# Performance work log

Hardware: AMD Instinct MI355X
Metric: run time of the kernel (lower is better)

The kernel has to match this reference:

```python
import jax, jax.numpy as jnp
import numpy as np

N_NODES = 100000


def sage_conv(x, src, dst, Wl, bl, Wr):
    # PyG SAGEConv (aggr='mean'): out = lin_l(mean_{j in N(i)} x_j) + lin_r(x_i)
    msg = x[src]                                                   # [E, d] gather
    agg = jax.ops.segment_sum(msg, dst, num_segments=N_NODES)      # [N, d]
    cnt = jax.ops.segment_sum(jnp.ones((src.shape[0], 1), x.dtype), dst,
                              num_segments=N_NODES)                # [N, 1]
    mean = agg / jnp.maximum(cnt, 1.0)
    return mean @ Wl + bl + x @ Wr


def setup_inputs() -> dict:
    key = jax.random.key(0)
    ks = jax.random.split(key, 9)
    N, E, D_IN = N_NODES, 3200000, 64
    x = jax.random.normal(ks[0], (N, D_IN), dtype=jnp.float32)
    edge_index = jax.random.randint(ks[1], (2, E), 0, N, dtype=jnp.int64)

    def glorot(k, fan_in, fan_out):
        lim = float(np.sqrt(6.0 / (fan_in + fan_out)))
        return jax.random.uniform(k, (fan_in, fan_out), jnp.float32, -lim, lim)

    return {
        "x": x,
        "edge_index": edge_index,
        "W1l": glorot(ks[2], D_IN, 64), "b1": jnp.zeros((64,), jnp.float32),
        "W1r": glorot(ks[3], D_IN, 64),
        "W2l": glorot(ks[4], 64, 32), "b2": jnp.zeros((32,), jnp.float32),
        "W2r": glorot(ks[5], 64, 32),
        "W3l": glorot(ks[6], 32, 1), "b3": jnp.zeros((1,), jnp.float32),
        "W3r": glorot(ks[7], 32, 1),
    }


def reference(x, edge_index, W1l, b1, W1r, W2l, b2, W2r, W3l, b3, W3r):
    src, dst = edge_index[0], edge_index[1]
    h = jax.nn.relu(sage_conv(x, src, dst, W1l, b1, W1r))   # dropout: eval mode (identity)
    h = jax.nn.relu(sage_conv(h, src, dst, W2l, b2, W2r))
    h = sage_conv(h, src, dst, W3l, b3, W3r)
    return jax.nn.sigmoid(h)                                # [N, 1]
```

## Files before the change

### kernel.cpp

```cpp
#include <hip/hip_runtime.h>
#include <math.h>

#define NN 100000
#define NB 391
#define BT 8192
#define CAP 12288

typedef float vfloat2 __attribute__((ext_vector_type(2)));
typedef short short8 __attribute__((ext_vector_type(8)));
typedef float floatx4 __attribute__((ext_vector_type(4)));

__device__ __forceinline__ unsigned short f2bf(float f) {
    unsigned int u = __float_as_uint(f);
    u += 0x7fffu + ((u >> 16) & 1u);
    return (unsigned short)(u >> 16);
}

__device__ __forceinline__ unsigned char f2fp8(float f) {
    const int p = __builtin_amdgcn_cvt_pk_fp8_f32(f, f, 0, false);
    return (unsigned char)(p & 0xFF);
}
template <bool HI>
__device__ __forceinline__ vfloat2 fp8pk2(unsigned int w) {
    return __builtin_amdgcn_cvt_pk_f32_fp8((int)w, HI);
}

template <int D_IN, int CL, int CR, int NPB, int FUSE_IN>
__global__ void __launch_bounds__(256)
mlp_mfma_kernel(const float* __restrict__ in0,
                const float* __restrict__ in1,
                const float* __restrict__ Wl,
                const float* __restrict__ Wr,
                const float* __restrict__ bias,
                unsigned char* __restrict__ yout,
                float* __restrict__ zout,
                int n_nodes) {
    constexpr int COLS = CL + CR;
    constexpr int CT = COLS / 16;
    constexpr int KT = D_IN / 32;
    constexpr int NT = NPB / 16;
    constexpr int KG = D_IN / 8;
    __shared__ short sA[NT * KT * 64 * 8];
    __shared__ short sB[CT * KT * 64 * 8];
    __shared__ float sBias[CR];
    const int t = threadIdx.x;
    const int node0 = blockIdx.x * NPB;

    for (int i = t; i < NPB * KG; i += 256) {
        const int nl = i / KG, kg = i % KG;
        const int n = node0 + nl;
        float v[8];
        if (n < n_nodes) {
            const float4* p = (const float4*)(in0 + (long long)n * D_IN + kg * 8);
            float4 a0 = p[0], a1 = p[1];
            if (FUSE_IN) {
                const float4* q = (const float4*)(in1 + (long long)n * D_IN + kg * 8);
                const float4 b0 = q[0], b1 = q[1];
                a0.x = fmaxf(a0.x + b0.x, 0.f); a0.y = fmaxf(a0.y + b0.y, 0.f);
                a0.z = fmaxf(a0.z + b0.z, 0.f); a0.w = fmaxf(a0.w + b0.w, 0.f);
                a1.x = fmaxf(a1.x + b1.x, 0.f); a1.y = fmaxf(a1.y + b1.y, 0.f);
                a1.z = fmaxf(a1.z + b1.z, 0.f); a1.w = fmaxf(a1.w + b1.w, 0.f);
            }
            v[0] = a0.x; v[1] = a0.y; v[2] = a0.z; v[3] = a0.w;
            v[4] = a1.x; v[5] = a1.y; v[6] = a1.z; v[7] = a1.w;
        } else {
#pragma unroll
            for (int j = 0; j < 8; ++j) v[j] = 0.f;
        }
        short8 s;
#pragma unroll
        for (int j = 0; j < 8; ++j) s[j] = (short)f2bf(v[j]);
        const int nt = nl >> 4, m = nl & 15, kt = kg >> 2, quad = kg & 3;
        ((short8*)sA)[(nt * KT + kt) * 64 + quad * 16 + m] = s;
    }
    for (int i = t; i < CT * KT * 64; i += 256) {
        const int ct = i / (KT * 64);
        const int rem = i % (KT * 64);
        const int kt = rem / 64, L = rem % 64;
        const int c = ct * 16 + (L & 15);
        const int k0 = kt * 32 + (L >> 4) * 8;
        short8 s;
#pragma unroll
        for (int j = 0; j < 8; ++j) {
            const int k = k0 + j;
            const float w = (c < CL) ? Wl[k * CL + c] : Wr[k * CR + (c - CL)];
            s[j] = (short)f2bf(w);
        }
        ((short8*)sB)[i] = s;
    }
    for (int i = t; i < CR; i += 256) sBias[i] = bias[i];
    __syncthreads();

    const int w = t >> 6, lane = t & 63;
    short8 Bf[CT][KT];
#pragma unroll
    for (int ct = 0; ct < CT; ++ct)
#pragma unroll
        for (int kt = 0; kt < KT; ++kt)
            Bf[ct][kt] = ((short8*)sB)[(ct * KT + kt) * 64 + lane];
    const int col = lane & 15, quad = lane >> 4;
#pragma unroll
    for (int nti = 0; nti < NT / 4; ++nti) {
        const int nt = w * (NT / 4) + nti;
        short8 A[KT];
#pragma unroll
        for (int kt = 0; kt < KT; ++kt)
            A[kt] = ((short8*)sA)[(nt * KT + kt) * 64 + lane];
        const int nodeb = node0 + nt * 16 + quad * 4;
#pragma unroll
        for (int ct = 0; ct < CT; ++ct) {
            floatx4 acc = {0.f, 0.f, 0.f, 0.f};
#pragma unroll
            for (int kt = 0; kt < KT; ++kt)
                acc = __builtin_amdgcn_mfma_f32_16x16x32_bf16(A[kt], Bf[ct][kt], acc, 0, 0, 0);
            const int gc = ct * 16 + col;
#pragma unroll
            for (int r = 0; r < 4; ++r) {
                const int node = nodeb + r;
                if (node < n_nodes) {
                    if (gc < CL) yout[(long long)node * CL + gc] = f2fp8(acc[r]);
                    else zout[(long long)node * CR + (gc - CL)] = acc[r] + sBias[gc - CL];
                }
            }
        }
    }
}

template <int D_IN>
__global__ void __launch_bounds__(256)
mlp3_kernel(const float* __restrict__ mean,
            const float* __restrict__ z,
            const float* __restrict__ W3l,
            const float* __restrict__ W3r,
            const float* __restrict__ b3,
            float* __restrict__ y,
            float* __restrict__ z3, int n_nodes) {
    __shared__ float swl[D_IN], swr[D_IN];
    const int t = threadIdx.x;
    if (t < D_IN) { swl[t] = W3l[t]; swr[t] = W3r[t]; }
    __syncthreads();
    const int n = blockIdx.x * 256 + t;
    if (n >= n_nodes) return;
    const float4* pm = (const float4*)(mean + (long long)n * D_IN);
    const float4* pz = (const float4*)(z + (long long)n * D_IN);
    float accl = 0.f, accr = 0.f;
#pragma unroll
    for (int q = 0; q < D_IN / 4; ++q) {
        const float4 m4 = pm[q];
        const float4 z4 = pz[q];
        const float h0 = fmaxf(m4.x + z4.x, 0.f);
        const float h1 = fmaxf(m4.y + z4.y, 0.f);
        const float h2 = fmaxf(m4.z + z4.z, 0.f);
        const float h3 = fmaxf(m4.w + z4.w, 0.f);
        accl += h0 * swl[4 * q] + h1 * swl[4 * q + 1] + h2 * swl[4 * q + 2] + h3 * swl[4 * q + 3];
        accr += h0 * swr[4 * q] + h1 * swr[4 * q + 1] + h2 * swr[4 * q + 2] + h3 * swr[4 * q + 3];
    }
    y[n] = accl;
    z3[n] = accr + b3[0];
}

__global__ void sigmoid_out_kernel(const float* __restrict__ mean,
                                   const float* __restrict__ z,
                                   float* __restrict__ out, int n) {
    const int i = blockIdx.x * 256 + threadIdx.x;
    if (i < n) out[i] = 1.0f / (1.0f + expf(-(mean[i] + z[i])));
}

__global__ void bucket_hist_kernel(const int* __restrict__ dst,
                                   int* __restrict__ bcnt, int n_edges) {
    __shared__ int lh[NB];
    for (int i = threadIdx.x; i < NB; i += 256) lh[i] = 0;
    __syncthreads();
    const int stride = gridDim.x * 256;
    for (int i = blockIdx.x * 256 + threadIdx.x; i < n_edges; i += stride)
        atomicAdd(&lh[dst[i] >> 8], 1);
    __syncthreads();
    for (int i = threadIdx.x; i < NB; i += 256)
        if (lh[i]) atomicAdd(&bcnt[i], lh[i]);
}

__global__ void __launch_bounds__(512)
bucket_scan_kernel(const int* __restrict__ bcnt, int* __restrict__ boffs,
                   int* __restrict__ bcursor) {
    __shared__ int s[512];
    const int t = threadIdx.x;
    const int v = (t < NB) ? bcnt[t] : 0;
    s[t] = v;
    __syncthreads();
    for (int off = 1; off < 512; off <<= 1) {
        const int tmp = (t >= off) ? s[t - off] : 0;
        __syncthreads();
        s[t] += tmp;
        __syncthreads();
    }
    const int excl = s[t] - v;
    if (t <= NB) boffs[t] = excl;
    if (t < NB) bcursor[t] = excl;
}

__global__ void __launch_bounds__(512)
bin_edges_kernel(const int* __restrict__ src, const int* __restrict__ dst,
                 int* __restrict__ bcursor, unsigned int* __restrict__ binned,
                 int n_edges) {
    __shared__ unsigned int stage[BT];
    __shared__ unsigned short sbkt[BT];
    __shared__ int lhist[512], lscan[512], lstart[512], gbase[512], lcur[512];
    const int t = threadIdx.x;
    const int e0 = blockIdx.x * BT;
    const int count = min(BT, n_edges - e0);
    lhist[t] = 0;
    __syncthreads();
    for (int i = t; i < count; i += 512) atomicAdd(&lhist[dst[e0 + i] >> 8], 1);
    __syncthreads();
    const int v = lhist[t];
    lscan[t] = v;
    __syncthreads();
    for (int off = 1; off < 512; off <<= 1) {
        const int tmp = (t >= off) ? lscan[t - off] : 0;
        __syncthreads();
        lscan[t] += tmp;
        __syncthreads();
    }
    const int excl = lscan[t] - v;
    lstart[t] = excl;
    lcur[t] = excl;
    if (t < NB && v > 0) gbase[t] = atomicAdd(&bcursor[t], v);
    __syncthreads();
    for (int i = t; i < count; i += 512) {
        const int d = dst[e0 + i];
        const int b = d >> 8;
        const int p = atomicAdd(&lcur[b], 1);
        stage[p] = (unsigned int)src[e0 + i] | ((unsigned int)(d & 255) << 17);
        sbkt[p] = (unsigned short)b;
    }
    __syncthreads();
    for (int i = t; i < count; i += 512) {
        const int b = sbkt[i];
        binned[gbase[b] + (i - lstart[b])] = stage[i];
    }
}

__global__ void __launch_bounds__(1024)
csr_sort_kernel(const unsigned int* __restrict__ binned,
                const int* __restrict__ boffs,
                int* __restrict__ ssrc, int* __restrict__ row_ptr,
                float* __restrict__ inv_deg, int n_nodes, int n_edges) {
    __shared__ int stage[CAP];
    __shared__ int hist[256];
    __shared__ int lexcl[256];
    __shared__ int lcur[256];
    const int t = threadIdx.x;
    const int b = blockIdx.x;
    const int s0 = boffs[b], s1 = boffs[b + 1];
    const int count = s1 - s0;
    if (t < 256) hist[t] = 0;
    __syncthreads();
    for (int i = t; i < count; i += 1024)
        atomicAdd(&hist[binned[s0 + i] >> 17], 1);
    __syncthreads();
    if (t < 256) lexcl[t] = hist[t];
    __syncthreads();
    for (int off = 1; off < 256; off <<= 1) {
        int tmp = 0;
        if (t < 256 && t >= off) tmp = lexcl[t - off];
        __syncthreads();
        if (t < 256) lexcl[t] += tmp;
        __syncthreads();
    }
    if (t < 256) {
        const int excl = lexcl[t] - hist[t];
        lcur[t] = excl;
        const int n = (b << 8) + t;
        if (n < n_nodes) {
            row_ptr[n] = s0 + excl;
            inv_deg[n] = 1.0f / (float)max(hist[t], 1);
        }
    }
    if (b == NB - 1 && t == 0) row_ptr[n_nodes] = n_edges;
    __syncthreads();
    for (int i = t; i < count; i += 1024) {
        const unsigned int v = binned[s0 + i];
        const int p = atomicAdd(&lcur[v >> 17], 1);
        if (p < CAP) stage[p] = (int)(v & 0x1FFFFu);
    }
    __syncthreads();
    for (int i = t; i < count; i += 1024) ssrc[s0 + i] = stage[i];
}

template <int D>
__global__ void agg_mean_fp8_kernel(const unsigned int* __restrict__ yb,
                                    const int* __restrict__ row_ptr,
                                    const int* __restrict__ ssrc,
                                    const float* __restrict__ inv_deg,
                                    float* __restrict__ mean, int n_nodes) {
    constexpr int G = D / 16;
    constexpr int NPB = 256 / G;
    const int g = threadIdx.x / G;
    const int lane = threadIdx.x % G;
    const int n = blockIdx.x * NPB + g;
    if (n >= n_nodes) return;
    const int s0 = row_ptr[n], s1 = row_ptr[n + 1];
    const uint4* yv = (const uint4*)yb;
    float acc[16];
#pragma unroll
    for (int i = 0; i < 16; ++i) acc[i] = 0.f;
    int e = s0;
    for (; e + 4 <= s1; e += 4) {
        uint4 v[4];
        v[0] = yv[(long long)ssrc[e] * G + lane];
        v[1] = yv[(long long)ssrc[e + 1] * G + lane];
        v[2] = yv[(long long)ssrc[e + 2] * G + lane];
        v[3] = yv[(long long)ssrc[e + 3] * G + lane];
#pragma unroll
        for (int q = 0; q < 4; ++q) {
            const unsigned int wx = v[q].x, wy = v[q].y, wz = v[q].z, ww = v[q].w;
            vfloat2 p;
            p = fp8pk2<false>(wx); acc[0]  += p.x; acc[1]  += p.y;
            p = fp8pk2<true>(wx);  acc[2]  += p.x; acc[3]  += p.y;
            p = fp8pk2<false>(wy); acc[4]  += p.x; acc[5]  += p.y;
            p = fp8pk2<true>(wy);  acc[6]  += p.x; acc[7]  += p.y;
            p = fp8pk2<false>(wz); acc[8]  += p.x; acc[9]  += p.y;
            p = fp8pk2<true>(wz);  acc[10] += p.x; acc[11] += p.y;
            p = fp8pk2<false>(ww); acc[12] += p.x; acc[13] += p.y;
            p = fp8pk2<true>(ww);  acc[14] += p.x; acc[15] += p.y;
        }
    }
    for (; e < s1; ++e) {
        const uint4 v = yv[(long long)ssrc[e] * G + lane];
        vfloat2 p;
        p = fp8pk2<false>(v.x); acc[0]  += p.x; acc[1]  += p.y;
        p = fp8pk2<true>(v.x);  acc[2]  += p.x; acc[3]  += p.y;
        p = fp8pk2<false>(v.y); acc[4]  += p.x; acc[5]  += p.y;
        p = fp8pk2<true>(v.y);  acc[6]  += p.x; acc[7]  += p.y;
        p = fp8pk2<false>(v.z); acc[8]  += p.x; acc[9]  += p.y;
        p = fp8pk2<true>(v.z);  acc[10] += p.x; acc[11] += p.y;
        p = fp8pk2<false>(v.w); acc[12] += p.x; acc[13] += p.y;
        p = fp8pk2<true>(v.w);  acc[14] += p.x; acc[15] += p.y;
    }
    const float inv = inv_deg[n];
    float4* mv = (float4*)mean;
    const long long base = (long long)n * (D / 4) + lane * 4;
#pragma unroll
    for (int q = 0; q < 4; ++q)
        mv[base + q] = make_float4(acc[4 * q] * inv, acc[4 * q + 1] * inv,
                                   acc[4 * q + 2] * inv, acc[4 * q + 3] * inv);
}

__global__ void agg_mean_d1_kernel(const float* __restrict__ y,
                                   const int* __restrict__ row_ptr,
                                   const int* __restrict__ ssrc,
                                   const float* __restrict__ inv_deg,
                                   float* __restrict__ mean, int n_nodes) {
    const int wave = threadIdx.x >> 6;
    const int lane = threadIdx.x & 63;
    const int n = blockIdx.x * 4 + wave;
    if (n >= n_nodes) return;
    const int s0 = row_ptr[n], s1 = row_ptr[n + 1];
    float acc = 0.f;
    for (int e = s0 + lane; e < s1; e += 64) acc += y[ssrc[e]];
    for (int off = 32; off > 0; off >>= 1) acc += __shfl_down(acc, off, 64);
    if (lane == 0) mean[n] = acc * inv_deg[n];
}

extern "C" void kernel_launch(void* const* d_in, const int* in_sizes, int n_in,
                              void* d_out, int out_size, void* d_ws, size_t ws_size,
                              hipStream_t stream) {
    const float* x = (const float*)d_in[0];
    const int* edge_index = (const int*)d_in[1];
    const float* W1l = (const float*)d_in[2];
    const float* b1  = (const float*)d_in[3];
    const float* W1r = (const float*)d_in[4];
    const float* W2l = (const float*)d_in[5];
    const float* b2  = (const float*)d_in[6];
    const float* W2r = (const float*)d_in[7];
    const float* W3l = (const float*)d_in[8];
    const float* b3  = (const float*)d_in[9];
    const float* W3r = (const float*)d_in[10];
    float* out = (float*)d_out;

    const int E = in_sizes[1] / 2;
    const int* src = edge_index;
    const int* dst = edge_index + E;

    float* bufY    = (float*)d_ws;
    float* meanB   = bufY + 32LL * NN;
    float* z1      = meanB + 64LL * NN;
    float* z2      = z1 + 64LL * NN;
    float* z3      = z2 + 32LL * NN;
    float* inv_deg = z3 + NN;
    int* bcnt      = (int*)(inv_deg + NN);
    int* boffs     = bcnt + NB;
    int* bcursor   = boffs + NB + 1;
    int* row_ptr   = bcursor + NB;
    int* ssrc      = row_ptr + NN + 1;
    unsigned int* binned = (unsigned int*)z1;

    const int ntiles = (E + BT - 1) / BT;

    (void)hipMemsetAsync(bcnt, 0, NB * sizeof(int), stream);
    bucket_hist_kernel<<<512, 256, 0, stream>>>(dst, bcnt, E);
    bucket_scan_kernel<<<1, 512, 0, stream>>>(bcnt, boffs, bcursor);
    bin_edges_kernel<<<ntiles, 512, 0, stream>>>(src, dst, bcursor, binned, E);
    csr_sort_kernel<<<NB, 1024, 0, stream>>>(binned, boffs, ssrc, row_ptr, inv_deg, NN, E);

    mlp_mfma_kernel<64, 64, 64, 128, 0><<<(NN + 127) / 128, 256, 0, stream>>>(
        x, nullptr, W1l, W1r, b1, (unsigned char*)bufY, z1, NN);
    agg_mean_fp8_kernel<64><<<(NN + 63) / 64, 256, 0, stream>>>(
        (const unsigned int*)bufY, row_ptr, ssrc, inv_deg, meanB, NN);

    mlp_mfma_kernel<64, 32, 32, 128, 1><<<(NN + 127) / 128, 256, 0, stream>>>(
        meanB, z1, W2l, W2r, b2, (unsigned char*)bufY, z2, NN);
    agg_mean_fp8_kernel<32><<<(NN + 127) / 128, 256, 0, stream>>>(
        (const unsigned int*)bufY, row_ptr, ssrc, inv_deg, meanB, NN);

    mlp3_kernel<32><<<(NN + 255) / 256, 256, 0, stream>>>(
        meanB, z2, W3l, W3r, b3, bufY, z3, NN);
    agg_mean_d1_kernel<<<(NN + 3) / 4, 256, 0, stream>>>(
        bufY, row_ptr, ssrc, inv_deg, meanB, NN);
    sigmoid_out_kernel<<<(NN + 255) / 256, 256, 0, stream>>>(meanB, z3, out, NN);
}
```

Baseline: 301.8 us.

## Split layer-1 aggregation into planar halves and fuse tail kernels

```diff
diff --git a/kernel.cpp b/kernel.cpp
--- a/kernel.cpp
+++ b/kernel.cpp
@@ -25,7 +25,19 @@
     return __builtin_amdgcn_cvt_pk_f32_fp8((int)w, HI);
 }
 
-template <int D_IN, int CL, int CR, int NPB, int FUSE_IN>
+__device__ __forceinline__ void fp8x16_acc(const uint4 v, float* acc) {
+    vfloat2 p;
+    p = fp8pk2<false>(v.x); acc[0]  += p.x; acc[1]  += p.y;
+    p = fp8pk2<true>(v.x);  acc[2]  += p.x; acc[3]  += p.y;
+    p = fp8pk2<false>(v.y); acc[4]  += p.x; acc[5]  += p.y;
+    p = fp8pk2<true>(v.y);  acc[6]  += p.x; acc[7]  += p.y;
+    p = fp8pk2<false>(v.z); acc[8]  += p.x; acc[9]  += p.y;
+    p = fp8pk2<true>(v.z);  acc[10] += p.x; acc[11] += p.y;
+    p = fp8pk2<false>(v.w); acc[12] += p.x; acc[13] += p.y;
+    p = fp8pk2<true>(v.w);  acc[14] += p.x; acc[15] += p.y;
+}
+
+template <int D_IN, int CL, int CR, int NPB, int FUSE_IN, int YPLANAR>
 __global__ void __launch_bounds__(256)
 mlp_mfma_kernel(const float* __restrict__ in0,
                 const float* __restrict__ in1,
@@ -118,52 +130,147 @@
             for (int r = 0; r < 4; ++r) {
                 const int node = nodeb + r;
                 if (node < n_nodes) {
-                    if (gc < CL) yout[(long long)node * CL + gc] = f2fp8(acc[r]);
-                    else zout[(long long)node * CR + (gc - CL)] = acc[r] + sBias[gc - CL];
+                    if (gc < CL) {
+                        if (YPLANAR) {
+                            const int plane = gc >> 5;
+                            yout[(long long)plane * NN * 32 + (long long)node * 32 + (gc & 31)] = f2fp8(acc[r]);
+                        } else {
+                            yout[(long long)node * CL + gc] = f2fp8(acc[r]);
+                        }
+                    } else {
+                        zout[(long long)node * CR + (gc - CL)] = acc[r] + sBias[gc - CL];
+                    }
                 }
             }
         }
     }
 }
 
-template <int D_IN>
+template <int HALF>
+__global__ void __launch_bounds__(128)
+agg64_half_kernel(const unsigned int* __restrict__ yb,
+                  const int* __restrict__ row_ptr,
+                  const int* __restrict__ ssrc,
+                  const float* __restrict__ inv_deg,
+                  float* __restrict__ mean, int n_nodes) {
+    const int g = threadIdx.x >> 1;
+    const int lane = threadIdx.x & 1;
+    const int n = blockIdx.x * 64 + g;
+    if (n >= n_nodes) return;
+    const int s0 = row_ptr[n], s1 = row_ptr[n + 1];
+    const uint4* yv = (const uint4*)yb;
+    const long long pbase = (long long)HALF * NN * 2;
+    float acc[16];
+#pragma unroll
+    for (int i = 0; i < 16; ++i) acc[i] = 0.f;
+    int e = s0;
+    for (; e + 4 <= s1; e += 4) {
+        const int i0 = __builtin_nontemporal_load(ssrc + e);
+        const int i1 = __builtin_nontemporal_load(ssrc + e + 1);
+        const int i2 = __builtin_nontemporal_load(ssrc + e + 2);
+        const int i3 = __builtin_nontemporal_load(ssrc + e + 3);
+        const uint4 v0 = yv[pbase + (long long)i0 * 2 + lane];
+        const uint4 v1 = yv[pbase + (long long)i1 * 2 + lane];
+        const uint4 v2 = yv[pbase + (long long)i2 * 2 + lane];
+        const uint4 v3 = yv[pbase + (long long)i3 * 2 + lane];
+        fp8x16_acc(v0, acc); fp8x16_acc(v1, acc);
+        fp8x16_acc(v2, acc); fp8x16_acc(v3, acc);
+    }
+    for (; e < s1; ++e) {
+        const int i0 = __builtin_nontemporal_load(ssrc + e);
+        fp8x16_acc(yv[pbase + (long long)i0 * 2 + lane], acc);
+    }
+    const float inv = inv_deg[n];
+    float4* mv = (float4*)mean;
+    const long long base = (long long)n * 16 + HALF * 8 + lane * 4;
+#pragma unroll
+    for (int q = 0; q < 4; ++q)
+        mv[base + q] = make_float4(acc[4 * q] * inv, acc[4 * q + 1] * inv,
+                                   acc[4 * q + 2] * inv, acc[4 * q + 3] * inv);
+}
+
 __global__ void __launch_bounds__(256)
-mlp3_kernel(const float* __restrict__ mean,
-            const float* __restrict__ z,
-            const float* __restrict__ W3l,
-            const float* __restrict__ W3r,
-            const float* __restrict__ b3,
-            float* __restrict__ y,
-            float* __restrict__ z3, int n_nodes) {
-    __shared__ float swl[D_IN], swr[D_IN];
-    const int t = threadIdx.x;
-    if (t < D_IN) { swl[t] = W3l[t]; swr[t] = W3r[t]; }
-    __syncthreads();
-    const int n = blockIdx.x * 256 + t;
+agg32_mlp3_kernel(const unsigned int* __restrict__ yb,
+                  const int* __restrict__ row_ptr,
+                  const int* __restrict__ ssrc,
+                  const float* __restrict__ inv_deg,
+                  const float* __restrict__ z2,
+                  const float* __restrict__ W3l,
+                  const float* __restrict__ W3r,
+                  const float* __restrict__ b3,
+                  float* __restrict__ y3,
+                  float* __restrict__ z3, int n_nodes) {
+    const int g = threadIdx.x >> 1;
+    const int lane = threadIdx.x & 1;
+    const int n = blockIdx.x * 128 + g;
     if (n >= n_nodes) return;
-    const float4* pm = (const float4*)(mean + (long long)n * D_IN);
-    const float4* pz = (const float4*)(z + (long long)n * D_IN);
+    float wl[16], wr[16];
+#pragma unroll
+    for (int i = 0; i < 16; ++i) {
+        wl[i] = W3l[lane * 16 + i];
+        wr[i] = W3r[lane * 16 + i];
+    }
+    const int s0 = row_ptr[n], s1 = row_ptr[n + 1];
+    const uint4* yv = (const uint4*)yb;
+    float acc[16];
+#pragma unroll
+    for (int i = 0; i < 16; ++i) acc[i] = 0.f;
+    int e = s0;
+    for (; e + 4 <= s1; e += 4) {
+        const int i0 = __builtin_nontemporal_load(ssrc + e);
+        const int i1 = __builtin_nontemporal_load(ssrc + e + 1);
+        const int i2 = __builtin_nontemporal_load(ssrc + e + 2);
+        const int i3 = __builtin_nontemporal_load(ssrc + e + 3);
+        const uint4 v0 = yv[(long long)i0 * 2 + lane];
+        const uint4 v1 = yv[(long long)i1 * 2 + lane];
+        const uint4 v2 = yv[(long long)i2 * 2 + lane];
+        const uint4 v3 = yv[(long long)i3 * 2 + lane];
+        fp8x16_acc(v0, acc); fp8x16_acc(v1, acc);
+        fp8x16_acc(v2, acc); fp8x16_acc(v3, acc);
+    }
+    for (; e < s1; ++e) {
+        const int i0 = __builtin_nontemporal_load(ssrc + e);
+        fp8x16_acc(yv[(long long)i0 * 2 + lane], acc);
+    }
+    const float inv = inv_deg[n];
+    const float4* pz = (const float4*)(z2 + (long long)n * 32 + lane * 16);
     float accl = 0.f, accr = 0.f;
 #pragma unroll
-    for (int q = 0; q < D_IN / 4; ++q) {
-        const float4 m4 = pm[q];
+    for (int q = 0; q < 4; ++q) {
         const float4 z4 = pz[q];
-        const float h0 = fmaxf(m4.x + z4.x, 0.f);
-        const float h1 = fmaxf(m4.y + z4.y, 0.f);
-        const float h2 = fmaxf(m4.z + z4.z, 0.f);
-        const float h3 = fmaxf(m4.w + z4.w, 0.f);
-        accl += h0 * swl[4 * q] + h1 * swl[4 * q + 1] + h2 * swl[4 * q + 2] + h3 * swl[4 * q + 3];
-        accr += h0 * swr[4 * q] + h1 * swr[4 * q + 1] + h2 * swr[4 * q + 2] + h3 * swr[4 * q + 3];
-    }
-    y[n] = accl;
-    z3[n] = accr + b3[0];
-}
-
-__global__ void sigmoid_out_kernel(const float* __restrict__ mean,
-                                   const float* __restrict__ z,
-                                   float* __restrict__ out, int n) {
-    const int i = blockIdx.x * 256 + threadIdx.x;
-    if (i < n) out[i] = 1.0f / (1.0f + expf(-(mean[i] + z[i])));
+        const float h0 = fmaxf(acc[4 * q]     * inv + z4.x, 0.f);
+        const float h1 = fmaxf(acc[4 * q + 1] * inv + z4.y, 0.f);
+        const float h2 = fmaxf(acc[4 * q + 2] * inv + z4.z, 0.f);
+        const float h3 = fmaxf(acc[4 * q + 3] * inv + z4.w, 0.f);
+        accl += h0 * wl[4 * q] + h1 * wl[4 * q + 1] + h2 * wl[4 * q + 2] + h3 * wl[4 * q + 3];
+        accr += h0 * wr[4 * q] + h1 * wr[4 * q + 1] + h2 * wr[4 * q + 2] + h3 * wr[4 * q + 3];
+    }
+    accl += __shfl_xor(accl, 1, 64);
+    accr += __shfl_xor(accr, 1, 64);
+    if (lane == 0) {
+        y3[n] = accl;
+        z3[n] = accr + b3[0];
+    }
+}
+
+__global__ void agg_d1_sig_kernel(const float* __restrict__ y,
+                                  const int* __restrict__ row_ptr,
+                                  const int* __restrict__ ssrc,
+                                  const float* __restrict__ inv_deg,
+                                  const float* __restrict__ z3,
+                                  float* __restrict__ out, int n_nodes) {
+    const int wave = threadIdx.x >> 6;
+    const int lane = threadIdx.x & 63;
+    const int n = blockIdx.x * 4 + wave;
+    if (n >= n_nodes) return;
+    const int s0 = row_ptr[n], s1 = row_ptr[n + 1];
+    float acc = 0.f;
+    for (int e = s0 + lane; e < s1; e += 64) acc += y[ssrc[e]];
+    for (int off = 32; off > 0; off >>= 1) acc += __shfl_down(acc, off, 64);
+    if (lane == 0) {
+        const float v = acc * inv_deg[n] + z3[n];
+        out[n] = 1.0f / (1.0f + expf(-v));
+    }
 }
 
 __global__ void bucket_hist_kernel(const int* __restrict__ dst,
@@ -285,81 +392,6 @@
     }
     __syncthreads();
     for (int i = t; i < count; i += 1024) ssrc[s0 + i] = stage[i];
-}
-
-template <int D>
-__global__ void agg_mean_fp8_kernel(const unsigned int* __restrict__ yb,
-                                    const int* __restrict__ row_ptr,
-                                    const int* __restrict__ ssrc,
-                                    const float* __restrict__ inv_deg,
-                                    float* __restrict__ mean, int n_nodes) {
-    constexpr int G = D / 16;
-    constexpr int NPB = 256 / G;
-    const int g = threadIdx.x / G;
-    const int lane = threadIdx.x % G;
-    const int n = blockIdx.x * NPB + g;
-    if (n >= n_nodes) return;
-    const int s0 = row_ptr[n], s1 = row_ptr[n + 1];
-    const uint4* yv = (const uint4*)yb;
-    float acc[16];
-#pragma unroll
-    for (int i = 0; i < 16; ++i) acc[i] = 0.f;
-    int e = s0;
-    for (; e + 4 <= s1; e += 4) {
-        uint4 v[4];
-        v[0] = yv[(long long)ssrc[e] * G + lane];
-        v[1] = yv[(long long)ssrc[e + 1] * G + lane];
-        v[2] = yv[(long long)ssrc[e + 2] * G + lane];
-        v[3] = yv[(long long)ssrc[e + 3] * G + lane];
-#pragma unroll
-        for (int q = 0; q < 4; ++q) {
-            const unsigned int wx = v[q].x, wy = v[q].y, wz = v[q].z, ww = v[q].w;
-            vfloat2 p;
-            p = fp8pk2<false>(wx); acc[0]  += p.x; acc[1]  += p.y;
-            p = fp8pk2<true>(wx);  acc[2]  += p.x; acc[3]  += p.y;
-            p = fp8pk2<false>(wy); acc[4]  += p.x; acc[5]  += p.y;
-            p = fp8pk2<true>(wy);  acc[6]  += p.x; acc[7]  += p.y;
-            p = fp8pk2<false>(wz); acc[8]  += p.x; acc[9]  += p.y;
-            p = fp8pk2<true>(wz);  acc[10] += p.x; acc[11] += p.y;
-            p = fp8pk2<false>(ww); acc[12] += p.x; acc[13] += p.y;
-            p = fp8pk2<true>(ww);  acc[14] += p.x; acc[15] += p.y;
-        }
-    }
-    for (; e < s1; ++e) {
-        const uint4 v = yv[(long long)ssrc[e] * G + lane];
-        vfloat2 p;
-        p = fp8pk2<false>(v.x); acc[0]  += p.x; acc[1]  += p.y;
-        p = fp8pk2<true>(v.x);  acc[2]  += p.x; acc[3]  += p.y;
-        p = fp8pk2<false>(v.y); acc[4]  += p.x; acc[5]  += p.y;
-        p = fp8pk2<true>(v.y);  acc[6]  += p.x; acc[7]  += p.y;
-        p = fp8pk2<false>(v.z); acc[8]  += p.x; acc[9]  += p.y;
-        p = fp8pk2<true>(v.z);  acc[10] += p.x; acc[11] += p.y;
-        p = fp8pk2<false>(v.w); acc[12] += p.x; acc[13] += p.y;
-        p = fp8pk2<true>(v.w);  acc[14] += p.x; acc[15] += p.y;
-    }
-    const float inv = inv_deg[n];
-    float4* mv = (float4*)mean;
-    const long long base = (long long)n * (D / 4) + lane * 4;
-#pragma unroll
-    for (int q = 0; q < 4; ++q)
-        mv[base + q] = make_float4(acc[4 * q] * inv, acc[4 * q + 1] * inv,
-                                   acc[4 * q + 2] * inv, acc[4 * q + 3] * inv);
-}
-
-__global__ void agg_mean_d1_kernel(const float* __restrict__ y,
-                                   const int* __restrict__ row_ptr,
-                                   const int* __restrict__ ssrc,
-                                   const float* __restrict__ inv_deg,
-                                   float* __restrict__ mean, int n_nodes) {
-    const int wave = threadIdx.x >> 6;
-    const int lane = threadIdx.x & 63;
-    const int n = blockIdx.x * 4 + wave;
-    if (n >= n_nodes) return;
-    const int s0 = row_ptr[n], s1 = row_ptr[n + 1];
-    float acc = 0.f;
-    for (int e = s0 + lane; e < s1; e += 64) acc += y[ssrc[e]];
-    for (int off = 32; off > 0; off >>= 1) acc += __shfl_down(acc, off, 64);
-    if (lane == 0) mean[n] = acc * inv_deg[n];
 }
 
 extern "C" void kernel_launch(void* const* d_in, const int* in_sizes, int n_in,
@@ -403,19 +435,20 @@
     bin_edges_kernel<<<ntiles, 512, 0, stream>>>(src, dst, bcursor, binned, E);
     csr_sort_kernel<<<NB, 1024, 0, stream>>>(binned, boffs, ssrc, row_ptr, inv_deg, NN, E);
 
-    mlp_mfma_kernel<64, 64, 64, 128, 0><<<(NN + 127) / 128, 256, 0, stream>>>(
+    mlp_mfma_kernel<64, 64, 64, 128, 0, 1><<<(NN + 127) / 128, 256, 0, stream>>>(
         x, nullptr, W1l, W1r, b1, (unsigned char*)bufY, z1, NN);
-    agg_mean_fp8_kernel<64><<<(NN + 63) / 64, 256, 0, stream>>>(
+    agg64_half_kernel<0><<<(NN + 63) / 64, 128, 0, stream>>>(
         (const unsigned int*)bufY, row_ptr, ssrc, inv_deg, meanB, NN);
-
-    mlp_mfma_kernel<64, 32, 32, 128, 1><<<(NN + 127) / 128, 256, 0, stream>>>(
+    agg64_half_kernel<1><<<(NN + 63) / 64, 128, 0, stream>>>(
+        (const unsigned int*)bufY, row_ptr, ssrc, inv_deg, meanB, NN);
+
+    mlp_mfma_kernel<64, 32, 32, 128, 1, 0><<<(NN + 127) / 128, 256, 0, stream>>>(
         meanB, z1, W2l, W2r, b2, (unsigned char*)bufY, z2, NN);
-    agg_mean_fp8_kernel<32><<<(NN + 127) / 128, 256, 0, stream>>>(
-        (const unsigned int*)bufY, row_ptr, ssrc, inv_deg, meanB, NN);
-
-    mlp3_kernel<32><<<(NN + 255) / 256, 256, 0, stream>>>(
-        meanB, z2, W3l, W3r, b3, bufY, z3, NN);
-    agg_mean_d1_kernel<<<(NN + 3) / 4, 256, 0, stream>>>(
-        bufY, row_ptr, ssrc, inv_deg, meanB, NN);
-    sigmoid_out_kernel<<<(NN + 255) / 256, 256, 0, stream>>>(meanB, z3, out, NN);
-}
+
+    float* y3 = meanB;
+    agg32_mlp3_kernel<<<(NN + 127) / 128, 256, 0, stream>>>(
+        (const unsigned int*)bufY, row_ptr, ssrc, inv_deg, z2, W3l, W3r, b3, y3, z3, NN);
+
+    agg_d1_sig_kernel<<<(NN + 3) / 4, 256, 0, stream>>>(
+        y3, row_ptr, ssrc, inv_deg, z3, out, NN);
+}
```

Result: slower. 340.7 us (+12.9%).
